# Performance work log

Hardware: AMD Instinct MI355X
Metric: run time of the kernel (lower is better)

## Reference

```python
import jax, jax.numpy as jnp
import numpy as np

N = 6144          # atoms (~300 residues)
K = 6             # sequence-separation bins (k_vals clamped to 0..5)
T = 85            # RASP 'all' atom types
D = 21            # distance bins -> max_d = 20 A
NBRE_NT_EXCLU = 2 # exclude pairs with residue separation <= 2
N_RES = 307


def setup_inputs() -> dict:
    key = jax.random.key(0)
    k1, k2, k3, k4, k5 = jax.random.split(key, 5)
    # coords scaled so pair distances populate the 0..20 A bin range
    coords = jax.random.normal(k1, (N, 3), jnp.float32) * 5.0
    # atoms grouped by residue -> sorted residue ids
    res_ids = jnp.sort(jax.random.randint(k2, (N,), 0, N_RES)).astype(jnp.int32)
    types = jax.random.randint(k3, (N,), 0, T).astype(jnp.int32)
    types = jnp.where(jax.random.uniform(k4, (N,)) < 0.02, jnp.int32(-1), types)
    pot_tensor = jax.random.normal(k5, (K, T, T, D), jnp.float32) * 0.5
    return {"coords": coords, "res_ids": res_ids, "types": types, "pot_tensor": pot_tensor}


def reference(coords, res_ids, types, pot_tensor):
    n = coords.shape[0]
    # static upper-triangular pair indices (i < j), as in torch.triu_indices(offset=1)
    ii_np, jj_np = np.triu_indices(n, k=1)
    ii = jnp.asarray(ii_np, jnp.int32)
    jj = jnp.asarray(jj_np, jnp.int32)

    sep = jnp.abs(res_ids[ii] - res_ids[jj])                       # [P]
    mask = (sep > NBRE_NT_EXCLU) & (types[ii] != -1) & (types[jj] != -1)

    diff = coords[ii] - coords[jj]                                 # [P,3]
    dists = jnp.sqrt(jnp.sum(diff * diff, axis=1)) + 1e-8          # [P]

    k_vals = jnp.clip(sep - 1, 0, 5)
    max_d = pot_tensor.shape[3] - 1
    d0 = jnp.floor(jnp.clip(dists, 0, max_d)).astype(jnp.int32)
    d1 = jnp.minimum(d0 + 1, max_d)
    alpha = dists - d0.astype(dists.dtype)

    # masked pairs may carry type -1; redirect their gather to index 0
    # (their contribution is zeroed by `mask` below, matching torch semantics)
    ti = jnp.where(mask, types[ii], 0)
    tj = jnp.where(mask, types[jj], 0)

    e0 = pot_tensor[k_vals, ti, tj, d0]                            # [P] 4D gather
    e1 = pot_tensor[k_vals, ti, tj, d1]

    contrib = ((1.0 - alpha) * e0 + alpha * e1 - 2.7)
    contrib = contrib * (dists < max_d).astype(contrib.dtype) * mask.astype(contrib.dtype)
    return jnp.sum(contrib)
```

## Files before the change

### kernel.cpp

```cpp
#include <hip/hip_runtime.h>


#define T_TYPES 85
#define D_BINS 21
#define KSTRIDE (T_TYPES * T_TYPES * D_BINS)
#define NKEYS 86
#define TILE 128
#define PAIR_THREADS 256
#define JCHUNK 64
#define MAXN 8192

__device__ float4 g_sorted[MAXN];

__global__ __launch_bounds__(1024) void sort_kernel(const float* __restrict__ coords,
                                                    const int* __restrict__ res_ids,
                                                    const int* __restrict__ types,
                                                    int n, int npad,
                                                    float* __restrict__ out) {
    __shared__ int hist[NKEYS];
    __shared__ int offs[NKEYS];
    int tid = threadIdx.x;
    if (tid < NKEYS) hist[tid] = 0;
    if (tid == 0) *out = 0.0f;
    __syncthreads();
    int n4 = n >> 2;
    for (int i = tid; i < n4; i += 1024) {
        int4 tv = ((const int4*)types)[i];
        atomicAdd(&hist[(tv.x < 0) ? (NKEYS - 1) : tv.x], 1);
        atomicAdd(&hist[(tv.y < 0) ? (NKEYS - 1) : tv.y], 1);
        atomicAdd(&hist[(tv.z < 0) ? (NKEYS - 1) : tv.z], 1);
        atomicAdd(&hist[(tv.w < 0) ? (NKEYS - 1) : tv.w], 1);
    }
    for (int i = (n4 << 2) + tid; i < n; i += 1024) {
        int t = types[i];
        atomicAdd(&hist[(t < 0) ? (NKEYS - 1) : t], 1);
    }
    __syncthreads();
    if (tid < NKEYS) {
        int s = 0;
#pragma unroll 1
        for (int k = 0; k < NKEYS; ++k) {
            int h = hist[k];
            s += (k < tid) ? h : 0;
        }
        offs[tid] = s;
    }
    __syncthreads();
    for (int i = tid; i < n; i += 1024) {
        int t = types[i];
        int inv = (t < 0);
        int key = inv ? (NKEYS - 1) : t;
        int pos = atomicAdd(&offs[key], 1);
        float4 v;
        if (inv) {
            v.x = 1e8f * (float)(i + 1);
            v.y = 0.0f;
            v.z = 0.0f;
            v.w = __int_as_float(0);
        } else {
            v.x = coords[3 * i + 0];
            v.y = coords[3 * i + 1];
            v.z = coords[3 * i + 2];
            v.w = __int_as_float((res_ids[i] << 11) | (t * D_BINS));
        }
        g_sorted[pos] = v;
    }
    for (int i = n + tid; i < npad; i += 1024) {
        float4 v;
        v.x = 1e8f * (float)(i + 1);
        v.y = 0.0f;
        v.z = 0.0f;
        v.w = __int_as_float(0);
        g_sorted[i] = v;
    }
}

template <bool DIAG>
__device__ __forceinline__ float tile_accum(float4 mine, int resi, int tbase,
                                            int j0, int p, int q0,
                                            const float* __restrict__ pot) {
    float acc = 0.0f;
#pragma unroll 8
    for (int u = 0; u < JCHUNK; ++u) {
        int jj = j0 + u;
        float4 o = g_sorted[q0 + jj];
        float dx = mine.x - o.x;
        float dy = mine.y - o.y;
        float dz = mine.z - o.z;
        float d2 = __builtin_fmaf(dx, dx, __builtin_fmaf(dy, dy, dz * dz));
        float dist = __builtin_amdgcn_sqrtf(d2) + 1e-8f;

        int packj = __float_as_int(o.w);
        int resj = packj >> 11;
        int kj21 = packj & 0x7FF;
        int sep = resi - resj;
        sep = (sep < 0) ? -sep : sep;

        int valid = (sep > 2) & (dist < 20.0f);
        if (DIAG) valid &= ((q0 + jj) > p);

        int k = sep - 1;
        k = (k > 5) ? 5 : k;
        int d0i = (int)dist;
        d0i = (d0i > 19) ? 19 : d0i;
        float alpha = dist - (float)d0i;

        int idx = k * KSTRIDE + (tbase + kj21 + d0i);
        idx = valid ? idx : 0;
        float e0 = pot[idx];
        float e1 = pot[idx + 1];
        float val = __builtin_fmaf(alpha, e1 - e0, e0) - 2.7f;
        acc += valid ? val : 0.0f;
    }
    return acc;
}

__global__ __launch_bounds__(PAIR_THREADS, 6) void pair_kernel(const float* __restrict__ pot,
                                                               int nt,
                                                               float* __restrict__ out) {
    __shared__ float wsum[PAIR_THREADS / 64];

    int b = blockIdx.x;
    int bi = (int)((2.0 * nt + 1.0 -
                    sqrt((2.0 * nt + 1.0) * (2.0 * nt + 1.0) - 8.0 * (double)b)) * 0.5);
    if (bi < 0) bi = 0;
    if (bi > nt - 1) bi = nt - 1;
    while ((bi + 1) * nt - ((bi + 1) * bi) / 2 <= b) ++bi;
    while (bi * nt - (bi * (bi - 1)) / 2 > b) --bi;
    int bj = bi + (b - (bi * nt - (bi * (bi - 1)) / 2));

    int tid = threadIdx.x;
    int ilane = tid & (TILE - 1);
    int chunk = tid >> 7;
    int q0 = bj * TILE;
    int p = bi * TILE + ilane;

    float4 mine = g_sorted[p];

    int packi = __float_as_int(mine.w);
    int resi = packi >> 11;
    int tbase = (packi & 0x7FF) * T_TYPES;
    int j0 = chunk * JCHUNK;

    float acc;
    if (bi == bj)
        acc = tile_accum<true>(mine, resi, tbase, j0, p, q0, pot);
    else
        acc = tile_accum<false>(mine, resi, tbase, j0, p, q0, pot);

#pragma unroll
    for (int off = 32; off > 0; off >>= 1)
        acc += __shfl_down(acc, off, 64);
    int wave = tid >> 6;
    if ((tid & 63) == 0) wsum[wave] = acc;
    __syncthreads();
    if (tid == 0) {
        float s = wsum[0] + wsum[1] + wsum[2] + wsum[3];
        atomicAdd(out, s);
    }
}

extern "C" void kernel_launch(void* const* d_in, const int* in_sizes, int n_in,
                              void* d_out, int out_size, void* d_ws, size_t ws_size,
                              hipStream_t stream) {
    const float* coords = (const float*)d_in[0];
    const int* res_ids = (const int*)d_in[1];
    const int* types   = (const int*)d_in[2];
    const float* pot   = (const float*)d_in[3];
    int n = in_sizes[1];
    float* out = (float*)d_out;

    int nt = (n + TILE - 1) / TILE;
    int npad = nt * TILE;

    sort_kernel<<<1, 1024, 0, stream>>>(coords, res_ids, types, n, npad, out);

    int nblocks = nt * (nt + 1) / 2;
    pair_kernel<<<nblocks, PAIR_THREADS, 0, stream>>>(pot, nt, out);
}
```

Before: 98.89 us.

## Split single-block counting sort into multi-block histogram and scatter kernels

Replaces the one-block 1024-thread type sort with two kernels: a per-block histogram written to a global partial table, then a scatter kernel where each block computes its own prefix offsets from all partials. This spreads the preprocessing across many CUs instead of serializing it on one block. It adds an extra kernel launch and redundant per-block prefix computations over the partial table, and with N=6144 only 24 blocks are used.

```diff
diff --git a/kernel.cpp b/kernel.cpp
--- a/kernel.cpp
+++ b/kernel.cpp
@@ -9,48 +9,61 @@
 #define PAIR_THREADS 256
 #define JCHUNK 64
 #define MAXN 8192
+#define MAXHB 32
 
 __device__ float4 g_sorted[MAXN];
+__device__ int g_part[MAXHB][NKEYS];
 
-__global__ __launch_bounds__(1024) void sort_kernel(const float* __restrict__ coords,
-                                                    const int* __restrict__ res_ids,
-                                                    const int* __restrict__ types,
-                                                    int n, int npad,
-                                                    float* __restrict__ out) {
+__global__ __launch_bounds__(256) void hist_kernel(const int* __restrict__ types,
+                                                   int n, float* __restrict__ out) {
     __shared__ int hist[NKEYS];
-    __shared__ int offs[NKEYS];
-    int tid = threadIdx.x;
+    int tid = threadIdx.x, b = blockIdx.x;
     if (tid < NKEYS) hist[tid] = 0;
-    if (tid == 0) *out = 0.0f;
+    if (b == 0 && tid == 0) *out = 0.0f;
     __syncthreads();
-    int n4 = n >> 2;
-    for (int i = tid; i < n4; i += 1024) {
-        int4 tv = ((const int4*)types)[i];
-        atomicAdd(&hist[(tv.x < 0) ? (NKEYS - 1) : tv.x], 1);
-        atomicAdd(&hist[(tv.y < 0) ? (NKEYS - 1) : tv.y], 1);
-        atomicAdd(&hist[(tv.z < 0) ? (NKEYS - 1) : tv.z], 1);
-        atomicAdd(&hist[(tv.w < 0) ? (NKEYS - 1) : tv.w], 1);
-    }
-    for (int i = (n4 << 2) + tid; i < n; i += 1024) {
+    int i = b * 256 + tid;
+    if (i < n) {
         int t = types[i];
         atomicAdd(&hist[(t < 0) ? (NKEYS - 1) : t], 1);
+    }
+    __syncthreads();
+    if (tid < NKEYS) g_part[b][tid] = hist[tid];
+}
+
+__global__ __launch_bounds__(256) void scatter_kernel(const float* __restrict__ coords,
+                                                      const int* __restrict__ res_ids,
+                                                      const int* __restrict__ types,
+                                                      int n, int nhb, int npad) {
+    __shared__ int base[NKEYS];
+    __shared__ int tot[NKEYS];
+    int tid = threadIdx.x, b = blockIdx.x;
+    if (tid < NKEYS) {
+        int t = 0, mine = 0;
+        for (int bb = 0; bb < nhb; ++bb) {
+            int h = g_part[bb][tid];
+            t += h;
+            mine += (bb < b) ? h : 0;
+        }
+        tot[tid] = t;
+        base[tid] = mine;
     }
     __syncthreads();
     if (tid < NKEYS) {
         int s = 0;
 #pragma unroll 1
         for (int k = 0; k < NKEYS; ++k) {
-            int h = hist[k];
-            s += (k < tid) ? h : 0;
+            int tk = tot[k];
+            s += (k < tid) ? tk : 0;
         }
-        offs[tid] = s;
+        base[tid] += s;
     }
     __syncthreads();
-    for (int i = tid; i < n; i += 1024) {
+    int i = b * 256 + tid;
+    if (i < n) {
         int t = types[i];
         int inv = (t < 0);
         int key = inv ? (NKEYS - 1) : t;
-        int pos = atomicAdd(&offs[key], 1);
+        int pos = atomicAdd(&base[key], 1);
         float4 v;
         if (inv) {
             v.x = 1e8f * (float)(i + 1);
@@ -64,8 +77,7 @@
             v.w = __int_as_float((res_ids[i] << 11) | (t * D_BINS));
         }
         g_sorted[pos] = v;
-    }
-    for (int i = n + tid; i < npad; i += 1024) {
+    } else if (i < npad) {
         float4 v;
         v.x = 1e8f * (float)(i + 1);
         v.y = 0.0f;
@@ -172,8 +184,11 @@
 
     int nt = (n + TILE - 1) / TILE;
     int npad = nt * TILE;
+    int nhb = (n + 255) / 256;
+    int npadb = (npad + 255) / 256;
 
-    sort_kernel<<<1, 1024, 0, stream>>>(coords, res_ids, types, n, npad, out);
+    hist_kernel<<<nhb, 256, 0, stream>>>(types, n, out);
+    scatter_kernel<<<npadb, 256, 0, stream>>>(coords, res_ids, types, n, nhb, npad);
 
     int nblocks = nt * (nt + 1) / 2;
     pair_kernel<<<nblocks, PAIR_THREADS, 0, stream>>>(pot, nt, out);
```

Result: no change. 97.39 us (-1.5%).
